# Optimization experiments

Measured on AMD Instinct MI355X. Metric: run time of the kernel, lower is better.

## Reference

```python
import jax, jax.numpy as jnp
import numpy as np
from jax.ops import segment_sum

N_NODES = 50000
N_EDGES = 800000


def _gcn_layer(h, src, dst, W, b, norm_out, norm_in, activation):
    # DGL GraphConv, norm='both': scale by src out-deg^-1/2, transform, aggregate, scale by dst in-deg^-1/2
    h = h * norm_out[:, None]
    h = h @ W                              # transform first (out dim smaller) -> cheaper messages
    msg = h[src]                           # [E, d_out] irregular gather
    agg = segment_sum(msg, dst, num_segments=h.shape[0])  # [N, d_out] scatter-add
    out = agg * norm_in[:, None] + b
    if activation is not None:
        out = activation(out)
    return out


def setup_inputs() -> dict:
    key = jax.random.key(0)
    ks = jax.random.split(key, 6)
    feat = jax.random.normal(ks[0], (N_NODES, 256), dtype=jnp.float32)
    src = jax.random.randint(ks[1], (N_EDGES,), 0, N_NODES, dtype=jnp.int32)
    dst = jax.random.randint(ks[2], (N_EDGES,), 0, N_NODES, dtype=jnp.int32)
    W1 = jax.random.normal(ks[3], (256, 64), dtype=jnp.float32) * (1.0 / np.sqrt(256))
    b1 = jnp.zeros((64,), dtype=jnp.float32)
    W2 = jax.random.normal(ks[4], (64, 40), dtype=jnp.float32) * (1.0 / np.sqrt(64))
    b2 = jnp.zeros((40,), dtype=jnp.float32)
    return {"feat": feat, "src": src, "dst": dst, "W1": W1, "b1": b1, "W2": W2, "b2": b2}


def reference(feat, src, dst, W1, b1, W2, b2):
    n = feat.shape[0]
    ones = jnp.ones((src.shape[0],), dtype=feat.dtype)
    deg_out = segment_sum(ones, src, num_segments=n)
    deg_in = segment_sum(ones, dst, num_segments=n)
    # DGL clamps degrees to min 1 (allow_zero_in_degree=True)
    norm_out = jnp.maximum(deg_out, 1.0) ** -0.5
    norm_in = jnp.maximum(deg_in, 1.0) ** -0.5
    h = _gcn_layer(feat, src, dst, W1, b1, norm_out, norm_in, jax.nn.relu)
    # dropout is identity in inference
    h = _gcn_layer(h, src, dst, W2, b2, norm_out, norm_in, None)
    return h
```

## Files before the change

### kernel.cpp

```cpp
#include <hip/hip_runtime.h>
#include <stdint.h>

#define N_NODES 50000
#define N_EDGES 800000
#define D_IN    256
#define D_H     64
#define D_O     40

#define NB_H   256
#define NT_H   512
#define EPB    (N_EDGES / NB_H)
#define BINS_W 12500

typedef unsigned int u32;
typedef unsigned short u16;
typedef unsigned char u8;
typedef __bf16 bf16;
typedef __attribute__((ext_vector_type(8))) __bf16 bf16x8;
typedef __attribute__((ext_vector_type(4))) float f32x4;


__global__ void __launch_bounds__(NT_H) hist_both_kernel(const int* __restrict__ src,
                                                         const int* __restrict__ dst,
                                                         u32* __restrict__ part_s,
                                                         u32* __restrict__ part_d) {
    __shared__ u32 bins[BINS_W];
    const int gb = blockIdx.x;
    const int b = (gb < NB_H) ? gb : gb - NB_H;
    const int* __restrict__ idx = (gb < NB_H) ? src : dst;
    u32* __restrict__ part = (gb < NB_H) ? part_s : part_d;
    const int e0 = b * EPB;
    const int e1 = (e0 + EPB < N_EDGES) ? e0 + EPB : N_EDGES;
    for (int i = threadIdx.x; i < BINS_W; i += NT_H) bins[i] = 0;
    __syncthreads();
    for (int e = e0 + threadIdx.x; e < e1; e += NT_H) {
        int v = idx[e];
        atomicAdd(&bins[v >> 2], 1u << ((v & 3) * 8));
    }
    __syncthreads();
    for (int i = threadIdx.x; i < BINS_W; i += NT_H)
        part[(size_t)b * BINS_W + i] = bins[i];
}


#define SCAN_NB ((N_NODES + 255) / 256)

__global__ void norm_both_kernel(const u8* __restrict__ part_s8,
                                 u8* __restrict__ part_d8,
                                 float* __restrict__ norm_out,
                                 int* __restrict__ cnt_in,
                                 float* __restrict__ norm_in) {
    const int half = blockIdx.x < SCAN_NB ? 0 : 1;
    const int n = (blockIdx.x - half * SCAN_NB) * blockDim.x + threadIdx.x;
    if (n >= N_NODES) return;
    if (half == 0) {
        u32 acc = 0;
#pragma unroll 8
        for (int b = 0; b < NB_H; ++b) acc += part_s8[(size_t)b * N_NODES + n];
        norm_out[n] = rsqrtf(fmaxf((float)acc, 1.0f));
    } else {
        u32 acc = 0;
#pragma unroll 8
        for (int b = 0; b < NB_H; ++b) {
            size_t i = (size_t)b * N_NODES + n;
            u8 t = part_d8[i];
            part_d8[i] = (u8)acc;
            acc += t;
        }
        cnt_in[n] = (int)acc;
        norm_in[n] = rsqrtf(fmaxf((float)acc, 1.0f));
    }
}


__global__ void scan1_kernel(const int* __restrict__ cnt, int* __restrict__ start,
                             int* __restrict__ blocksum) {
    __shared__ int tmp[256];
    int i = blockIdx.x * 256 + threadIdx.x;
    int v = (i < N_NODES) ? cnt[i] : 0;
    tmp[threadIdx.x] = v;
    __syncthreads();
    for (int off = 1; off < 256; off <<= 1) {
        int t = (threadIdx.x >= off) ? tmp[threadIdx.x - off] : 0;
        __syncthreads();
        tmp[threadIdx.x] += t;
        __syncthreads();
    }
    if (i < N_NODES) start[i] = tmp[threadIdx.x] - v;
    if (threadIdx.x == 255) blocksum[blockIdx.x] = tmp[255];
}

__global__ void scan2_kernel(int* __restrict__ blocksum) {
    __shared__ int tmp[256];
    int v = (threadIdx.x < SCAN_NB) ? blocksum[threadIdx.x] : 0;
    tmp[threadIdx.x] = v;
    __syncthreads();
    for (int off = 1; off < 256; off <<= 1) {
        int t = (threadIdx.x >= off) ? tmp[threadIdx.x - off] : 0;
        __syncthreads();
        tmp[threadIdx.x] += t;
        __syncthreads();
    }
    blocksum[threadIdx.x] = tmp[threadIdx.x] - v;
}

__global__ void scan3_kernel(int* __restrict__ start, const int* __restrict__ blocksum) {
    int i = blockIdx.x * 256 + threadIdx.x;
    if (i < N_NODES) start[i] += blocksum[i >> 8];
    if (i == 0) start[N_NODES] = N_EDGES;
}


__global__ void __launch_bounds__(NT_H) scatter2_kernel(const int* __restrict__ src,
                                                        const int* __restrict__ dst,
                                                        const int* __restrict__ start,
                                                        const u8* __restrict__ off8,
                                                        u16* __restrict__ ssrc) {
    __shared__ u32 cur[BINS_W];
    const int b = blockIdx.x;
    const int e0 = b * EPB;
    const int e1 = (e0 + EPB < N_EDGES) ? e0 + EPB : N_EDGES;
    for (int i = threadIdx.x; i < BINS_W; i += NT_H) cur[i] = 0;
    __syncthreads();
    for (int e = e0 + threadIdx.x; e < e1; e += NT_H) {
        int d = dst[e];
        int sh = (d & 3) * 8;
        u32 old = atomicAdd(&cur[d >> 2], 1u << sh);
        int c = (int)((old >> sh) & 0xFFu);
        int pos = start[d] + (int)off8[(size_t)b * N_NODES + d] + c;
        ssrc[pos] = (u16)src[e];
    }
}


#define AST 40

__global__ void __launch_bounds__(256, 4) gemm1_kernel(const float* __restrict__ feat,
                                                       const float* __restrict__ W1,
                                                       const float* __restrict__ norm_out,
                                                       bf16* __restrict__ h1) {
    __shared__ __align__(16) bf16 Ah[2][64 * AST];
    __shared__ __align__(16) bf16 Al[2][64 * AST];
    __shared__ __align__(16) bf16 Wh[2][64 * AST];
    __shared__ __align__(16) bf16 Wl[2][64 * AST];

    const int tid = threadIdx.x;
    const int lane = tid & 63;
    const int wv = __builtin_amdgcn_readfirstlane(tid >> 6);
    const int n0 = blockIdx.x * 64;

    const int ar = tid >> 2;
    const int ak = (tid & 3) * 8;
    int nra = n0 + ar; if (nra >= N_NODES) nra = N_NODES - 1;
    const float* asrc = feat + (size_t)nra * D_IN + ak;

    const int wcol = tid & 63;
    const int wk0 = (tid >> 6) * 8;
    const float* wsrc = W1 + wcol;

    f32x4 acc[4];
#pragma unroll
    for (int ct = 0; ct < 4; ++ct) acc[ct] = (f32x4){0.f, 0.f, 0.f, 0.f};

    const int fr = lane & 15;
    const int fg = (lane >> 4) * 8;

    auto stageA = [&](int buf, int s) {
        float4 a0 = *(const float4*)(asrc + s * 32);
        float4 a1 = *(const float4*)(asrc + s * 32 + 4);
        float av[8] = {a0.x, a0.y, a0.z, a0.w, a1.x, a1.y, a1.z, a1.w};
        bf16x8 H, L;
#pragma unroll
        for (int j = 0; j < 8; ++j) {
            bf16 h = (bf16)av[j];
            H[j] = h;
            L[j] = (bf16)(av[j] - (float)h);
        }
        *(bf16x8*)&Ah[buf][ar * AST + ak] = H;
        *(bf16x8*)&Al[buf][ar * AST + ak] = L;
    };

    auto stageW = [&](int buf, int s) {
        float wv8[8];
#pragma unroll
        for (int j = 0; j < 8; ++j)
            wv8[j] = wsrc[(size_t)(s * 32 + wk0 + j) * D_H];
        bf16x8 H, L;
#pragma unroll
        for (int j = 0; j < 8; ++j) {
            bf16 h = (bf16)wv8[j];
            H[j] = h;
            L[j] = (bf16)(wv8[j] - (float)h);
        }
        *(bf16x8*)&Wh[buf][wcol * AST + wk0] = H;
        *(bf16x8*)&Wl[buf][wcol * AST + wk0] = L;
    };

    auto compute = [&](int buf) {
        bf16x8 ah = *(const bf16x8*)&Ah[buf][(wv * 16 + fr) * AST + fg];
        bf16x8 al = *(const bf16x8*)&Al[buf][(wv * 16 + fr) * AST + fg];
#pragma unroll
        for (int ct = 0; ct < 4; ++ct) {
            bf16x8 bh = *(const bf16x8*)&Wh[buf][(ct * 16 + fr) * AST + fg];
            bf16x8 bl = *(const bf16x8*)&Wl[buf][(ct * 16 + fr) * AST + fg];
            acc[ct] = __builtin_amdgcn_mfma_f32_16x16x32_bf16(ah, bh, acc[ct], 0, 0, 0);
            acc[ct] = __builtin_amdgcn_mfma_f32_16x16x32_bf16(al, bh, acc[ct], 0, 0, 0);
            acc[ct] = __builtin_amdgcn_mfma_f32_16x16x32_bf16(ah, bl, acc[ct], 0, 0, 0);
        }
    };

    stageA(0, 0);
    stageW(0, 0);
    __syncthreads();
#pragma unroll
    for (int s = 0; s < 8; ++s) {
        const int buf = s & 1;
        if (s < 7) {
            stageA(buf ^ 1, s + 1);
            stageW(buf ^ 1, s + 1);
        }
        compute(buf);
        __syncthreads();
    }

    const int orow = n0 + wv * 16 + (lane >> 4) * 4;
    const int ocol = lane & 15;
    float nrm[4];
#pragma unroll
    for (int r = 0; r < 4; ++r)
        nrm[r] = (orow + r < N_NODES) ? norm_out[orow + r] : 0.0f;
#pragma unroll
    for (int ct = 0; ct < 4; ++ct) {
#pragma unroll
        for (int r = 0; r < 4; ++r) {
            if (orow + r < N_NODES)
                h1[(size_t)(orow + r) * D_H + ct * 16 + ocol] = (bf16)(acc[ct][r] * nrm[r]);
        }
    }
}


__global__ void __launch_bounds__(256) agg1_kernel(const int* __restrict__ start,
                                                   const u16* __restrict__ ssrc,
                                                   const bf16* __restrict__ h1,
                                                   const float* __restrict__ norm_in,
                                                   const float* __restrict__ norm_out,
                                                   const float* __restrict__ b1,
                                                   bf16* __restrict__ g) {
    const int lane = threadIdx.x & 63;
    const int c = lane & 7;
    const int t = lane >> 3;
    const int n = (int)((blockIdx.x * blockDim.x + threadIdx.x) >> 6);
    if (n >= N_NODES) return;

    int beg = __builtin_amdgcn_readfirstlane(start[n]);
    int end = __builtin_amdgcn_readfirstlane(start[n + 1]);
    float acc[8];
#pragma unroll
    for (int j = 0; j < 8; ++j) acc[j] = 0.0f;

    for (int e = beg + t; e < end; e += 16) {
        int s0 = ssrc[e];
        bf16x8 v0 = *(const bf16x8*)(h1 + (size_t)s0 * D_H + c * 8);
        if (e + 8 < end) {
            int s1 = ssrc[e + 8];
            bf16x8 v1 = *(const bf16x8*)(h1 + (size_t)s1 * D_H + c * 8);
#pragma unroll
            for (int j = 0; j < 8; ++j) acc[j] += (float)v1[j];
        }
#pragma unroll
        for (int j = 0; j < 8; ++j) acc[j] += (float)v0[j];
    }
#pragma unroll
    for (int j = 0; j < 8; ++j) {
        acc[j] += __shfl_xor(acc[j], 8);
        acc[j] += __shfl_xor(acc[j], 16);
        acc[j] += __shfl_xor(acc[j], 32);
    }
    if (t == 0) {
        float ni = norm_in[n], no = norm_out[n];
        float4 b0 = *(const float4*)&b1[c * 8];
        float4 b1v = *(const float4*)&b1[c * 8 + 4];
        bf16x8 r;
        r[0] = (bf16)(fmaxf(fmaf(acc[0], ni, b0.x), 0.f) * no);
        r[1] = (bf16)(fmaxf(fmaf(acc[1], ni, b0.y), 0.f) * no);
        r[2] = (bf16)(fmaxf(fmaf(acc[2], ni, b0.z), 0.f) * no);
        r[3] = (bf16)(fmaxf(fmaf(acc[3], ni, b0.w), 0.f) * no);
        r[4] = (bf16)(fmaxf(fmaf(acc[4], ni, b1v.x), 0.f) * no);
        r[5] = (bf16)(fmaxf(fmaf(acc[5], ni, b1v.y), 0.f) * no);
        r[6] = (bf16)(fmaxf(fmaf(acc[6], ni, b1v.z), 0.f) * no);
        r[7] = (bf16)(fmaxf(fmaf(acc[7], ni, b1v.w), 0.f) * no);
        *(bf16x8*)(g + (size_t)n * D_H + c * 8) = r;
    }
}


#define AST2 72

__global__ void __launch_bounds__(256, 4) gemm2_kernel(const bf16* __restrict__ g,
                                                       const float* __restrict__ W2,
                                                       bf16* __restrict__ h2) {
    __shared__ __align__(16) bf16 Ah[64 * AST2];
    __shared__ __align__(16) bf16 Wh[48 * AST2];
    __shared__ __align__(16) bf16 Wl[48 * AST2];

    const int tid = threadIdx.x;
    const int lane = tid & 63;
    const int wv = __builtin_amdgcn_readfirstlane(tid >> 6);
    const int n0 = blockIdx.x * 64;

    {
        const int ar = tid >> 2;
        const int ak = (tid & 3) * 16;
        int nra = n0 + ar; if (nra >= N_NODES) nra = N_NODES - 1;
        const bf16* asrc = g + (size_t)nra * D_H + ak;
        *(bf16x8*)&Ah[ar * AST2 + ak]     = *(const bf16x8*)(asrc);
        *(bf16x8*)&Ah[ar * AST2 + ak + 8] = *(const bf16x8*)(asrc + 8);
    }
    if (tid < 192) {
        const int col = tid >> 2;
        const int k0 = (tid & 3) * 16;
        float wv16[16];
#pragma unroll
        for (int j = 0; j < 16; ++j)
            wv16[j] = (col < D_O) ? W2[(size_t)(k0 + j) * D_O + col] : 0.0f;
        bf16x8 H0, L0, H1, L1;
#pragma unroll
        for (int j = 0; j < 8; ++j) {
            bf16 h = (bf16)wv16[j];
            H0[j] = h; L0[j] = (bf16)(wv16[j] - (float)h);
            bf16 hb = (bf16)wv16[j + 8];
            H1[j] = hb; L1[j] = (bf16)(wv16[j + 8] - (float)hb);
        }
        *(bf16x8*)&Wh[col * AST2 + k0] = H0;
        *(bf16x8*)&Wh[col * AST2 + k0 + 8] = H1;
        *(bf16x8*)&Wl[col * AST2 + k0] = L0;
        *(bf16x8*)&Wl[col * AST2 + k0 + 8] = L1;
    }
    __syncthreads();

    const int fr = lane & 15;
    const int fg = (lane >> 4) * 8;

    f32x4 acc[3];
#pragma unroll
    for (int ct = 0; ct < 3; ++ct) acc[ct] = (f32x4){0.f, 0.f, 0.f, 0.f};

#pragma unroll
    for (int s = 0; s < 2; ++s) {
        bf16x8 ah = *(const bf16x8*)&Ah[(wv * 16 + fr) * AST2 + s * 32 + fg];
#pragma unroll
        for (int ct = 0; ct < 3; ++ct) {
            bf16x8 bh = *(const bf16x8*)&Wh[(ct * 16 + fr) * AST2 + s * 32 + fg];
            bf16x8 bl = *(const bf16x8*)&Wl[(ct * 16 + fr) * AST2 + s * 32 + fg];
            acc[ct] = __builtin_amdgcn_mfma_f32_16x16x32_bf16(ah, bh, acc[ct], 0, 0, 0);
            acc[ct] = __builtin_amdgcn_mfma_f32_16x16x32_bf16(ah, bl, acc[ct], 0, 0, 0);
        }
    }

    const int orow = n0 + wv * 16 + (lane >> 4) * 4;
    const int ocol = lane & 15;
#pragma unroll
    for (int ct = 0; ct < 3; ++ct) {
        int col = ct * 16 + ocol;
        if (col < D_O) {
#pragma unroll
            for (int r = 0; r < 4; ++r) {
                if (orow + r < N_NODES)
                    h2[(size_t)(orow + r) * D_H + col] = (bf16)acc[ct][r];
            }
        }
    }
}


__global__ void __launch_bounds__(256) agg2_kernel(const int* __restrict__ start,
                                                   const u16* __restrict__ ssrc,
                                                   const bf16* __restrict__ h2,
                                                   const float* __restrict__ norm_in,
                                                   const float* __restrict__ b2,
                                                   float* __restrict__ out) {
    const int lane = threadIdx.x & 63;
    const int c = lane & 7;
    const int t = lane >> 3;
    const int n = (int)((blockIdx.x * blockDim.x + threadIdx.x) >> 6);
    if (n >= N_NODES) return;

    int beg = __builtin_amdgcn_readfirstlane(start[n]);
    int end = __builtin_amdgcn_readfirstlane(start[n + 1]);
    float acc[8];
#pragma unroll
    for (int j = 0; j < 8; ++j) acc[j] = 0.0f;

    for (int e = beg + t; e < end; e += 16) {
        int s0 = ssrc[e];
        bf16x8 v0 = *(const bf16x8*)(h2 + (size_t)s0 * D_H + c * 8);
        if (e + 8 < end) {
            int s1 = ssrc[e + 8];
            bf16x8 v1 = *(const bf16x8*)(h2 + (size_t)s1 * D_H + c * 8);
#pragma unroll
            for (int j = 0; j < 8; ++j) acc[j] += (float)v1[j];
        }
#pragma unroll
        for (int j = 0; j < 8; ++j) acc[j] += (float)v0[j];
    }
#pragma unroll
    for (int j = 0; j < 8; ++j) {
        acc[j] += __shfl_xor(acc[j], 8);
        acc[j] += __shfl_xor(acc[j], 16);
        acc[j] += __shfl_xor(acc[j], 32);
    }
    if (t == 0 && c < 5) {
        float ni = norm_in[n];
        float4 b0 = *(const float4*)&b2[c * 8];
        float4 b1v = *(const float4*)&b2[c * 8 + 4];
        float* op = out + (size_t)n * D_O + c * 8;
        *(float4*)(op) = make_float4(fmaf(acc[0], ni, b0.x), fmaf(acc[1], ni, b0.y),
                                     fmaf(acc[2], ni, b0.z), fmaf(acc[3], ni, b0.w));
        *(float4*)(op + 4) = make_float4(fmaf(acc[4], ni, b1v.x), fmaf(acc[5], ni, b1v.y),
                                         fmaf(acc[6], ni, b1v.z), fmaf(acc[7], ni, b1v.w));
    }
}


static inline char* alignup(char* p, size_t a) {
    return (char*)(((uintptr_t)p + a - 1) & ~(uintptr_t)(a - 1));
}

extern "C" void kernel_launch(void* const* d_in, const int* in_sizes, int n_in,
                              void* d_out, int out_size, void* d_ws, size_t ws_size,
                              hipStream_t stream) {
    const float* feat = (const float*)d_in[0];
    const int*   src  = (const int*)d_in[1];
    const int*   dst  = (const int*)d_in[2];
    const float* W1   = (const float*)d_in[3];
    const float* b1   = (const float*)d_in[4];
    const float* W2   = (const float*)d_in[5];
    const float* b2   = (const float*)d_in[6];
    float* out = (float*)d_out;

    char* p = alignup((char*)d_ws, 256);
    int*   cnt_in   = (int*)p;    p = alignup(p + N_NODES * 4, 256);
    int*   start    = (int*)p;    p = alignup(p + (N_NODES + 1) * 4, 256);
    int*   blocksum = (int*)p;    p = alignup(p + 256 * 4, 256);
    float* norm_out = (float*)p;  p = alignup(p + N_NODES * 4, 256);
    float* norm_in  = (float*)p;  p = alignup(p + N_NODES * 4, 256);
    u16*   ssrc     = (u16*)p;    p = alignup(p + N_EDGES * 2, 256);
    bf16*  h1       = (bf16*)p;   p = alignup(p + (size_t)N_NODES * D_H * 2, 256);
    bf16*  g        = (bf16*)p;   p = alignup(p + (size_t)N_NODES * D_H * 2, 256);
    u32*   part_s   = (u32*)p;    p = alignup(p + (size_t)NB_H * BINS_W * 4, 256);
    u32*   part_d   = (u32*)p;    p = alignup(p + (size_t)NB_H * BINS_W * 4, 256);
    bf16*  h2       = h1;

    hist_both_kernel<<<2 * NB_H, NT_H, 0, stream>>>(src, dst, part_s, part_d);
    norm_both_kernel<<<2 * SCAN_NB, 256, 0, stream>>>((const u8*)part_s, (u8*)part_d,
                                                      norm_out, cnt_in, norm_in);

    scan1_kernel<<<SCAN_NB, 256, 0, stream>>>(cnt_in, start, blocksum);
    scan2_kernel<<<1, 256, 0, stream>>>(blocksum);
    scan3_kernel<<<SCAN_NB, 256, 0, stream>>>(start, blocksum);

    scatter2_kernel<<<NB_H, NT_H, 0, stream>>>(src, dst, start, (const u8*)part_d, ssrc);

    gemm1_kernel<<<(N_NODES + 63) / 64, 256, 0, stream>>>(feat, W1, norm_out, h1);
    agg1_kernel<<<(N_NODES + 3) / 4, 256, 0, stream>>>(start, ssrc, h1, norm_in, norm_out, b1, g);

    gemm2_kernel<<<(N_NODES + 63) / 64, 256, 0, stream>>>(g, W2, h2);
    agg2_kernel<<<(N_NODES + 3) / 4, 256, 0, stream>>>(start, ssrc, h2, norm_in, b2, out);
}
```

Measured before the change: 121.6 us.

## Fuse in-degree scan into norm kernel, drop W1 low split, compact h2 to 40 cols

Merges the first-level prefix scan into the in-degree normalization kernel, which removes one launch and the cnt_in round trip through memory. Drops the low-order bf16 correction term for W1 in gemm1, which cuts one MFMA per tile along with the extra shared-memory staging at some cost in accuracy. Stores h2 with a 40-column stride in a separate buffer so agg2 gathers fewer bytes per edge and skips the unused column groups.

```diff
diff --git a/kernel.cpp b/kernel.cpp
--- a/kernel.cpp
+++ b/kernel.cpp
@@ -48,47 +48,46 @@
 __global__ void norm_both_kernel(const u8* __restrict__ part_s8,
                                  u8* __restrict__ part_d8,
                                  float* __restrict__ norm_out,
-                                 int* __restrict__ cnt_in,
-                                 float* __restrict__ norm_in) {
+                                 float* __restrict__ norm_in,
+                                 int* __restrict__ start,
+                                 int* __restrict__ blocksum) {
+    __shared__ int tmp[256];
     const int half = blockIdx.x < SCAN_NB ? 0 : 1;
-    const int n = (blockIdx.x - half * SCAN_NB) * blockDim.x + threadIdx.x;
-    if (n >= N_NODES) return;
     if (half == 0) {
+        const int n = blockIdx.x * 256 + threadIdx.x;
+        if (n >= N_NODES) return;
         u32 acc = 0;
 #pragma unroll 8
         for (int b = 0; b < NB_H; ++b) acc += part_s8[(size_t)b * N_NODES + n];
         norm_out[n] = rsqrtf(fmaxf((float)acc, 1.0f));
     } else {
+        const int blk = blockIdx.x - SCAN_NB;
+        const int n = blk * 256 + threadIdx.x;
         u32 acc = 0;
+        if (n < N_NODES) {
 #pragma unroll 8
-        for (int b = 0; b < NB_H; ++b) {
-            size_t i = (size_t)b * N_NODES + n;
-            u8 t = part_d8[i];
-            part_d8[i] = (u8)acc;
-            acc += t;
-        }
-        cnt_in[n] = (int)acc;
-        norm_in[n] = rsqrtf(fmaxf((float)acc, 1.0f));
-    }
-}
-
-
-__global__ void scan1_kernel(const int* __restrict__ cnt, int* __restrict__ start,
-                             int* __restrict__ blocksum) {
-    __shared__ int tmp[256];
-    int i = blockIdx.x * 256 + threadIdx.x;
-    int v = (i < N_NODES) ? cnt[i] : 0;
-    tmp[threadIdx.x] = v;
-    __syncthreads();
-    for (int off = 1; off < 256; off <<= 1) {
-        int t = (threadIdx.x >= off) ? tmp[threadIdx.x - off] : 0;
+            for (int b = 0; b < NB_H; ++b) {
+                size_t i = (size_t)b * N_NODES + n;
+                u8 t = part_d8[i];
+                part_d8[i] = (u8)acc;
+                acc += t;
+            }
+            norm_in[n] = rsqrtf(fmaxf((float)acc, 1.0f));
+        }
+        int v = (int)acc;
+        tmp[threadIdx.x] = v;
         __syncthreads();
-        tmp[threadIdx.x] += t;
-        __syncthreads();
-    }
-    if (i < N_NODES) start[i] = tmp[threadIdx.x] - v;
-    if (threadIdx.x == 255) blocksum[blockIdx.x] = tmp[255];
-}
+        for (int off = 1; off < 256; off <<= 1) {
+            int t = (threadIdx.x >= off) ? tmp[threadIdx.x - off] : 0;
+            __syncthreads();
+            tmp[threadIdx.x] += t;
+            __syncthreads();
+        }
+        if (n < N_NODES) start[n] = tmp[threadIdx.x] - v;
+        if (threadIdx.x == 255) blocksum[blk] = tmp[255];
+    }
+}
+
 
 __global__ void scan2_kernel(int* __restrict__ blocksum) {
     __shared__ int tmp[256];
@@ -142,7 +141,6 @@
     __shared__ __align__(16) bf16 Ah[2][64 * AST];
     __shared__ __align__(16) bf16 Al[2][64 * AST];
     __shared__ __align__(16) bf16 Wh[2][64 * AST];
-    __shared__ __align__(16) bf16 Wl[2][64 * AST];
 
     const int tid = threadIdx.x;
     const int lane = tid & 63;
@@ -185,15 +183,10 @@
 #pragma unroll
         for (int j = 0; j < 8; ++j)
             wv8[j] = wsrc[(size_t)(s * 32 + wk0 + j) * D_H];
-        bf16x8 H, L;
-#pragma unroll
-        for (int j = 0; j < 8; ++j) {
-            bf16 h = (bf16)wv8[j];
-            H[j] = h;
-            L[j] = (bf16)(wv8[j] - (float)h);
-        }
+        bf16x8 H;
+#pragma unroll
+        for (int j = 0; j < 8; ++j) H[j] = (bf16)wv8[j];
         *(bf16x8*)&Wh[buf][wcol * AST + wk0] = H;
-        *(bf16x8*)&Wl[buf][wcol * AST + wk0] = L;
     };
 
     auto compute = [&](int buf) {
@@ -202,10 +195,8 @@
 #pragma unroll
         for (int ct = 0; ct < 4; ++ct) {
             bf16x8 bh = *(const bf16x8*)&Wh[buf][(ct * 16 + fr) * AST + fg];
-            bf16x8 bl = *(const bf16x8*)&Wl[buf][(ct * 16 + fr) * AST + fg];
             acc[ct] = __builtin_amdgcn_mfma_f32_16x16x32_bf16(ah, bh, acc[ct], 0, 0, 0);
             acc[ct] = __builtin_amdgcn_mfma_f32_16x16x32_bf16(al, bh, acc[ct], 0, 0, 0);
-            acc[ct] = __builtin_amdgcn_mfma_f32_16x16x32_bf16(ah, bl, acc[ct], 0, 0, 0);
         }
     };
 
@@ -367,7 +358,7 @@
 #pragma unroll
             for (int r = 0; r < 4; ++r) {
                 if (orow + r < N_NODES)
-                    h2[(size_t)(orow + r) * D_H + col] = (bf16)acc[ct][r];
+                    h2[(size_t)(orow + r) * D_O + col] = (bf16)acc[ct][r];
             }
         }
     }
@@ -392,17 +383,19 @@
 #pragma unroll
     for (int j = 0; j < 8; ++j) acc[j] = 0.0f;
 
-    for (int e = beg + t; e < end; e += 16) {
-        int s0 = ssrc[e];
-        bf16x8 v0 = *(const bf16x8*)(h2 + (size_t)s0 * D_H + c * 8);
-        if (e + 8 < end) {
-            int s1 = ssrc[e + 8];
-            bf16x8 v1 = *(const bf16x8*)(h2 + (size_t)s1 * D_H + c * 8);
-#pragma unroll
-            for (int j = 0; j < 8; ++j) acc[j] += (float)v1[j];
-        }
-#pragma unroll
-        for (int j = 0; j < 8; ++j) acc[j] += (float)v0[j];
+    if (c < 5) {
+        for (int e = beg + t; e < end; e += 16) {
+            int s0 = ssrc[e];
+            bf16x8 v0 = *(const bf16x8*)(h2 + (size_t)s0 * D_O + c * 8);
+            if (e + 8 < end) {
+                int s1 = ssrc[e + 8];
+                bf16x8 v1 = *(const bf16x8*)(h2 + (size_t)s1 * D_O + c * 8);
+#pragma unroll
+                for (int j = 0; j < 8; ++j) acc[j] += (float)v1[j];
+            }
+#pragma unroll
+            for (int j = 0; j < 8; ++j) acc[j] += (float)v0[j];
+        }
     }
 #pragma unroll
     for (int j = 0; j < 8; ++j) {
@@ -440,7 +433,6 @@
     float* out = (float*)d_out;
 
     char* p = alignup((char*)d_ws, 256);
-    int*   cnt_in   = (int*)p;    p = alignup(p + N_NODES * 4, 256);
     int*   start    = (int*)p;    p = alignup(p + (N_NODES + 1) * 4, 256);
     int*   blocksum = (int*)p;    p = alignup(p + 256 * 4, 256);
     float* norm_out = (float*)p;  p = alignup(p + N_NODES * 4, 256);
@@ -448,15 +440,13 @@
     u16*   ssrc     = (u16*)p;    p = alignup(p + N_EDGES * 2, 256);
     bf16*  h1       = (bf16*)p;   p = alignup(p + (size_t)N_NODES * D_H * 2, 256);
     bf16*  g        = (bf16*)p;   p = alignup(p + (size_t)N_NODES * D_H * 2, 256);
+    bf16*  h2q     = (bf16*)p;    p = alignup(p + (size_t)N_NODES * D_O * 2, 256);
     u32*   part_s   = (u32*)p;    p = alignup(p + (size_t)NB_H * BINS_W * 4, 256);
     u32*   part_d   = (u32*)p;    p = alignup(p + (size_t)NB_H * BINS_W * 4, 256);
-    bf16*  h2       = h1;
 
     hist_both_kernel<<<2 * NB_H, NT_H, 0, stream>>>(src, dst, part_s, part_d);
     norm_both_kernel<<<2 * SCAN_NB, 256, 0, stream>>>((const u8*)part_s, (u8*)part_d,
-                                                      norm_out, cnt_in, norm_in);
-
-    scan1_kernel<<<SCAN_NB, 256, 0, stream>>>(cnt_in, start, blocksum);
+                                                      norm_out, norm_in, start, blocksum);
     scan2_kernel<<<1, 256, 0, stream>>>(blocksum);
     scan3_kernel<<<SCAN_NB, 256, 0, stream>>>(start, blocksum);
 
@@ -465,6 +455,6 @@
     gemm1_kernel<<<(N_NODES + 63) / 64, 256, 0, stream>>>(feat, W1, norm_out, h1);
     agg1_kernel<<<(N_NODES + 3) / 4, 256, 0, stream>>>(start, ssrc, h1, norm_in, norm_out, b1, g);
 
-    gemm2_kernel<<<(N_NODES + 63) / 64, 256, 0, stream>>>(g, W2, h2);
-    agg2_kernel<<<(N_NODES + 3) / 4, 256, 0, stream>>>(start, ssrc, h2, norm_in, b2, out);
-}
+    gemm2_kernel<<<(N_NODES + 63) / 64, 256, 0, stream>>>(g, W2, h2q);
+    agg2_kernel<<<(N_NODES + 3) / 4, 256, 0, stream>>>(start, ssrc, h2q, norm_in, b2, out);
+}
```

After: 113.6 us. -6.6%, faster.
